# Kernel tuning notes

Measured on AMD Instinct MI355X. Metric: run time of the kernel, lower is better.

## Reference

```python
import jax, jax.numpy as jnp
import numpy as np

SEQ_LEN = 1
INPUT = 2048
HIDDEN = 2048
CLASSES = 10
K = int(np.floor(np.sqrt(HIDDEN)))            # avgKernelSize = 45
NUM_EH = (HIDDEN - K) // K + 1                # 45 pooled features
LENGTHS = (32, 128, 512)                      # EHlengths (window sizes)
EST_DIM = NUM_EH * len(LENGTHS) * 2           # mean + variance per (feature, window)
B = 8192


def setup_inputs() -> dict:
    key = jax.random.key(0)
    ks = jax.random.split(key, 7)
    s = 1.0 / np.sqrt(HIDDEN)
    u = lambda k, shape: jax.random.uniform(k, shape, jnp.float32, -s, s)
    return {
        "x": jax.random.normal(ks[0], (B, SEQ_LEN, INPUT), jnp.float32),
        "W_ih": u(ks[1], (HIDDEN, INPUT)),
        "W_hh": u(ks[2], (HIDDEN, HIDDEN)),
        "b_ih": u(ks[3], (HIDDEN,)),
        "b_hh": u(ks[4], (HIDDEN,)),
        "W_lin": u(ks[5], (CLASSES, HIDDEN + EST_DIM)),
        "b_lin": u(ks[6], (CLASSES,)),
    }


def _sliding_stats(pooled):
    """Causal sliding-window mean/variance over the batch/stream axis.

    pooled: (B, F). Returns (B, F, J, 2) with [..., 0]=mean, [..., 1]=var.
    This is the exact quantity the VarEH exponential histograms approximate
    (streaming mean/variance over the last L elements added).
    """
    n = pooled.shape[0]
    cs = jnp.cumsum(pooled, axis=0)
    cs2 = jnp.cumsum(pooled * pooled, axis=0)
    idx = jnp.arange(n)
    outs = []
    for L in LENGTHS:  # small fixed set of window lengths
        zpad = jnp.zeros((L,) + pooled.shape[1:], pooled.dtype)
        cs_l = jnp.concatenate([zpad, cs], axis=0)[:n]
        cs2_l = jnp.concatenate([zpad, cs2], axis=0)[:n]
        cnt = jnp.minimum(idx + 1, L).astype(pooled.dtype)[:, None]
        m = (cs - cs_l) / cnt
        v = (cs2 - cs2_l) / cnt - m * m
        outs.append(jnp.stack([m, v], axis=-1))  # (B, F, 2)
    return jnp.stack(outs, axis=2)  # (B, F, J, 2)


def reference(x, W_ih, W_hh, b_ih, b_hh, W_lin, b_lin):
    b = x.shape[0]
    # Elman RNN, batch_first, h0 = 0. Precompute input projection for all steps.
    xw = jnp.einsum("bsi,hi->bsh", x, W_ih) + b_ih + b_hh  # (B, S, H)

    def step(h, xt):
        h = jnp.tanh(xt + h @ W_hh.T)
        return h, h

    h0 = jnp.zeros((b, HIDDEN), x.dtype)
    _, hs = jax.lax.scan(step, h0, jnp.swapaxes(xw, 0, 1))  # (S, B, H)
    rnn_out = hs[-1]  # (B, H); with seq_len=1 this equals squeeze(rnn_out)

    # AvgPool1d(kernel=K, stride=K) over hidden dim -> (B, NUM_EH)
    pooled = rnn_out[:, : NUM_EH * K].reshape(b, NUM_EH, K).mean(axis=-1)

    # Streaming mean/var estimates across the batch stream (VarEH semantics)
    est = _sliding_stats(pooled).reshape(b, EST_DIM)

    lin_in = jnp.concatenate([rnn_out, est], axis=1)  # (B, H + EST_DIM)
    logits = lin_in @ W_lin.T + b_lin
    return jax.nn.softmax(logits, axis=1)
```

## Files before the change

### kernel.cpp

```cpp
#include <hip/hip_runtime.h>
#include <hip/hip_bf16.h>
#include <math.h>

typedef short s16x8 __attribute__((ext_vector_type(8)));
typedef float f32x4 __attribute__((ext_vector_type(4)));

__device__ inline unsigned short f2bf(float x) {
    unsigned int u = __float_as_uint(x);
    unsigned int r = (u + 0x7fffu + ((u >> 16) & 1u)) >> 16;
    return (unsigned short)r;
}
__device__ inline float bf2f(unsigned short u) {
    return __uint_as_float(((unsigned int)u) << 16);
}

__device__ inline float fast_tanh(float x) {
    float e = __expf(2.0f * x);
    return 1.0f - 2.0f * __builtin_amdgcn_rcpf(e + 1.0f);
}

__global__ void cvtprep_kernel(const float* __restrict__ x,
                               const float* __restrict__ W_ih,
                               const float* __restrict__ W_lin,
                               unsigned short* __restrict__ xb,
                               unsigned short* __restrict__ wb,
                               unsigned short* __restrict__ wlb) {
    int blk = blockIdx.x;
    int tid = threadIdx.x;
    if (blk < 16384) {
        int i = blk * 256 + tid;
        float4 v = ((const float4*)x)[i];
        ushort4 o; o.x = f2bf(v.x); o.y = f2bf(v.y); o.z = f2bf(v.z); o.w = f2bf(v.w);
        ((ushort4*)xb)[i] = o;
    } else if (blk < 20480) {
        int i = (blk - 16384) * 256 + tid;
        float4 v = ((const float4*)W_ih)[i];
        ushort4 o; o.x = f2bf(v.x); o.y = f2bf(v.y); o.z = f2bf(v.z); o.w = f2bf(v.w);
        ((ushort4*)wb)[i] = o;
    } else {
        int idx = (blk - 20480) * 256 + tid;
        if (idx < 37376) {
            int c = idx / 2336, k = idx - c * 2336;
            float v = (c < 10 && k < 2318) ? W_lin[c * 2318 + k] : 0.f;
            wlb[idx] = f2bf(v);
        }
    }
}

__global__ __launch_bounds__(256) void gemm_tanh_kernel(
    const unsigned short* __restrict__ A, const unsigned short* __restrict__ Bm,
    const float* __restrict__ b_ih, const float* __restrict__ b_hh,
    unsigned short* __restrict__ Hb)
{
    __shared__ unsigned short As[128 * 32];
    __shared__ unsigned short Bs[128 * 32];

    const int tid  = threadIdx.x;
    const int lane = tid & 63;
    const int wave = tid >> 6;
    const int row0 = blockIdx.x * 128;
    const int col0 = blockIdx.y * 128;
    const int wr = (wave >> 1) * 64;
    const int wc = (wave & 1) * 64;
    const int quad = lane >> 4;
    const int mrow = lane & 15;

    f32x4 acc[4][4];
#pragma unroll
    for (int i = 0; i < 4; ++i)
#pragma unroll
        for (int j = 0; j < 4; ++j)
            acc[i][j] = f32x4{0.f, 0.f, 0.f, 0.f};

    for (int k0 = 0; k0 < 2048; k0 += 32) {
        __syncthreads();
#pragma unroll
        for (int i = 0; i < 2; ++i) {
            int t = i * 256 + tid;
            int r = t >> 2, c = t & 3;
            int cg = c ^ ((r >> 1) & 3);
            const unsigned short* gp = A + (size_t)(row0 + r) * 2048 + k0 + cg * 8;
            __builtin_amdgcn_global_load_lds(
                (const __attribute__((address_space(1))) void*)gp,
                (__attribute__((address_space(3))) void*)(&As[t * 8]), 16, 0, 0);
        }
#pragma unroll
        for (int i = 0; i < 2; ++i) {
            int t = i * 256 + tid;
            int r = t >> 2, c = t & 3;
            int cg = c ^ ((r >> 1) & 3);
            const unsigned short* gp = Bm + (size_t)(col0 + r) * 2048 + k0 + cg * 8;
            __builtin_amdgcn_global_load_lds(
                (const __attribute__((address_space(1))) void*)gp,
                (__attribute__((address_space(3))) void*)(&Bs[t * 8]), 16, 0, 0);
        }
        __syncthreads();

        s16x8 af[4], bfr[4];
#pragma unroll
        for (int i = 0; i < 4; ++i) {
            int R = wr + i * 16 + mrow;
            int slot = quad ^ ((R >> 1) & 3);
            af[i] = *(const s16x8*)(&As[R * 32 + slot * 8]);
        }
#pragma unroll
        for (int j = 0; j < 4; ++j) {
            int R = wc + j * 16 + mrow;
            int slot = quad ^ ((R >> 1) & 3);
            bfr[j] = *(const s16x8*)(&Bs[R * 32 + slot * 8]);
        }
#pragma unroll
        for (int i = 0; i < 4; ++i)
#pragma unroll
            for (int j = 0; j < 4; ++j)
                acc[i][j] = __builtin_amdgcn_mfma_f32_16x16x32_bf16(
                    af[i], bfr[j], acc[i][j], 0, 0, 0);
    }

    float bias[4];
#pragma unroll
    for (int j = 0; j < 4; ++j) {
        int gc = col0 + wc + j * 16 + mrow;
        bias[j] = b_ih[gc] + b_hh[gc];
    }
#pragma unroll
    for (int i = 0; i < 4; ++i) {
#pragma unroll
        for (int r = 0; r < 4; ++r) {
            int grow = row0 + wr + i * 16 + quad * 4 + r;
#pragma unroll
            for (int j = 0; j < 4; ++j) {
                int gc = col0 + wc + j * 16 + mrow;
                float v = acc[i][j][r] + bias[j];
                Hb[(size_t)grow * 2048 + gc] = f2bf(fast_tanh(v));
            }
        }
    }
}

__global__ __launch_bounds__(256) void pool_kernel(
    const unsigned short* __restrict__ Hb, float* __restrict__ pooled_t) {
    __shared__ unsigned short hs[8 * 2048];
    __shared__ float outs[45 * 8];
    int b0 = blockIdx.x * 8;
    int tid = threadIdx.x;
    const ushort4* src = (const ushort4*)(Hb + (size_t)b0 * 2048);
    ushort4* dst = (ushort4*)hs;
    for (int i = tid; i < 4096; i += 256) dst[i] = src[i];
    __syncthreads();
    for (int o = tid; o < 360; o += 256) {
        int f = o % 45, r = o / 45;
        const unsigned short* row = hs + r * 2048 + f * 45;
        float s = 0.f;
#pragma unroll
        for (int k = 0; k < 45; ++k) s += bf2f(row[k]);
        outs[f * 8 + r] = s * (1.0f / 45.0f);
    }
    __syncthreads();
    for (int o = tid; o < 360; o += 256) {
        int f = o >> 3, r = o & 7;
        pooled_t[f * 8192 + b0 + r] = outs[o];
    }
}

__global__ __launch_bounds__(256) void scan_kernel(
    const float* __restrict__ pooled_t,
    float* __restrict__ cs_t, float* __restrict__ cs2_t) {
    __shared__ float t1[256], t2[256];
    int f = blockIdx.x;
    int tid = threadIdx.x;
    const float* p = pooled_t + f * 8192;
    int base = tid * 32;
    float loc[32];
    float s1 = 0.f, s2 = 0.f;
#pragma unroll
    for (int i = 0; i < 32; ++i) {
        float v = p[base + i];
        loc[i] = v; s1 += v; s2 += v * v;
    }
    t1[tid] = s1; t2[tid] = s2;
    __syncthreads();
    for (int d = 1; d < 256; d <<= 1) {
        float a1 = (tid >= d) ? t1[tid - d] : 0.f;
        float a2 = (tid >= d) ? t2[tid - d] : 0.f;
        __syncthreads();
        t1[tid] += a1; t2[tid] += a2;
        __syncthreads();
    }
    float r1 = t1[tid] - s1, r2 = t2[tid] - s2;
    float* c1 = cs_t + f * 8192;
    float* c2 = cs2_t + f * 8192;
#pragma unroll
    for (int i = 0; i < 32; ++i) {
        float v = loc[i];
        r1 += v; r2 += v * v;
        c1[base + i] = r1; c2[base + i] = r2;
    }
}

#define ESTRIDE 290
__global__ __launch_bounds__(256) void final_kernel(
    const unsigned short* __restrict__ Hb,
    const float* __restrict__ cs_t, const float* __restrict__ cs2_t,
    const unsigned short* __restrict__ Wb, const float* __restrict__ b_lin,
    float* __restrict__ out) {
    __shared__ unsigned short Es[32 * ESTRIDE];
    __shared__ float comb[2 * 16 * 17];
    int tid = threadIdx.x;
    int lane = tid & 63;
    int wave = tid >> 6;
    int b0 = blockIdx.x * 32;

    for (int i = tid; i < 135 * 32; i += 256) {
        int fj = i >> 5, r = i & 31;
        int f = fj / 3, j = fj - 3 * f;
        int b = b0 + r;
        int L = (j == 0) ? 32 : (j == 1) ? 128 : 512;
        const float* c1 = cs_t + f * 8192;
        const float* c2 = cs2_t + f * 8192;
        float a1 = c1[b], a2 = c2[b];
        float p1 = 0.f, p2 = 0.f;
        if (b >= L) { p1 = c1[b - L]; p2 = c2[b - L]; }
        float cnt = (float)((b + 1 < L) ? (b + 1) : L);
        float m = (a1 - p1) / cnt;
        float v = (a2 - p2) / cnt - m * m;
        int d0 = f * 6 + j * 2;
        Es[r * ESTRIDE + d0]     = f2bf(m);
        Es[r * ESTRIDE + d0 + 1] = f2bf(v);
    }
    for (int i = tid; i < 32 * 18; i += 256) {
        int r = i / 18, d = 270 + i % 18;
        Es[r * ESTRIDE + d] = 0;
    }
    __syncthreads();

    const int t = wave >> 1;
    const int kh = wave & 1;
    const int quad = lane >> 4;
    const int mrow = lane & 15;
    const int rowt = b0 + t * 16;

    f32x4 acc = f32x4{0.f, 0.f, 0.f, 0.f};
    const unsigned short* arow = Hb + (size_t)(rowt + mrow) * 2048 + kh * 1024 + quad * 8;
    const unsigned short* brow = Wb + (size_t)mrow * 2336 + kh * 1024 + quad * 8;
#pragma unroll 4
    for (int k = 0; k < 1024; k += 32) {
        s16x8 a = *(const s16x8*)(arow + k);
        s16x8 b = *(const s16x8*)(brow + k);
        acc = __builtin_amdgcn_mfma_f32_16x16x32_bf16(a, b, acc, 0, 0, 0);
    }
    if (kh) {
        const unsigned short* erow = Es + (t * 16 + mrow) * ESTRIDE + quad * 8;
        const unsigned short* wrow = Wb + (size_t)mrow * 2336 + 2048 + quad * 8;
#pragma unroll
        for (int k = 0; k < 288; k += 32) {
            s16x8 a = *(const s16x8*)(erow + k);
            s16x8 b = *(const s16x8*)(wrow + k);
            acc = __builtin_amdgcn_mfma_f32_16x16x32_bf16(a, b, acc, 0, 0, 0);
        }
    }

    float* cb = comb + t * 272;
    if (kh == 0) {
#pragma unroll
        for (int r = 0; r < 4; ++r) cb[(quad * 4 + r) * 17 + mrow] = acc[r];
    }
    __syncthreads();
    if (kh == 1) {
#pragma unroll
        for (int r = 0; r < 4; ++r) cb[(quad * 4 + r) * 17 + mrow] += acc[r];
    }
    __syncthreads();

    if (tid < 32) {
        const float* base = comb + (tid >> 4) * 272 + (tid & 15) * 17;
        float lg[10];
        float mx = -1e30f;
#pragma unroll
        for (int c = 0; c < 10; ++c) {
            lg[c] = base[c] + b_lin[c];
            mx = fmaxf(mx, lg[c]);
        }
        float s = 0.f;
#pragma unroll
        for (int c = 0; c < 10; ++c) { lg[c] = expf(lg[c] - mx); s += lg[c]; }
        float inv = 1.0f / s;
#pragma unroll
        for (int c = 0; c < 10; ++c) out[(size_t)(b0 + tid) * 10 + c] = lg[c] * inv;
    }
}

extern "C" void kernel_launch(void* const* d_in, const int* in_sizes, int n_in,
                              void* d_out, int out_size, void* d_ws, size_t ws_size,
                              hipStream_t stream) {
    const float* x     = (const float*)d_in[0];
    const float* W_ih  = (const float*)d_in[1];
    const float* b_ih  = (const float*)d_in[3];
    const float* b_hh  = (const float*)d_in[4];
    const float* W_lin = (const float*)d_in[5];
    const float* b_lin = (const float*)d_in[6];
    float* out = (float*)d_out;

    char* ws = (char*)d_ws;
    unsigned short* xb  = (unsigned short*)(ws);
    unsigned short* wb  = (unsigned short*)(ws + 33554432);
    unsigned short* Hb  = (unsigned short*)(ws + 41943040);
    float* pooled_t     = (float*)(ws + 75497472);
    float* cs_t         = (float*)(ws + 76972032);
    float* cs2_t        = (float*)(ws + 78446592);
    unsigned short* wlb = (unsigned short*)(ws + 79921152);

    cvtprep_kernel<<<20626, 256, 0, stream>>>(x, W_ih, W_lin, xb, wb, wlb);
    dim3 ggrid(64, 16);
    gemm_tanh_kernel<<<ggrid, 256, 0, stream>>>(xb, wb, b_ih, b_hh, Hb);
    pool_kernel<<<1024, 256, 0, stream>>>(Hb, pooled_t);
    scan_kernel<<<45, 256, 0, stream>>>(pooled_t, cs_t, cs2_t);
    final_kernel<<<256, 256, 0, stream>>>(Hb, cs_t, cs2_t, wlb, b_lin, out);
}
```

Baseline: 253.8 us.

## Fuse fp32-to-bf16 conversion of x into the GEMM load path

Removes the separate pass that converted the 64MB fp32 input x to bf16 in workspace. The GEMM now loads fp32 x directly into registers, converts to bf16 and stores to LDS, while W_ih is still pre-converted. The grid is transposed so the 16 column blocks sharing the same rows of x run adjacently, which improves L2 reuse of the now twice-as-large fp32 A tiles. The cost is synchronous register-staged loads instead of async global_load_lds, plus conversion ALU work inside the main loop.

```diff
diff --git a/kernel.cpp b/kernel.cpp
--- a/kernel.cpp
+++ b/kernel.cpp
@@ -10,6 +10,9 @@
     unsigned int r = (u + 0x7fffu + ((u >> 16) & 1u)) >> 16;
     return (unsigned short)r;
 }
+__device__ inline unsigned int f2bf2(float lo, float hi) {
+    return ((unsigned int)f2bf(hi) << 16) | (unsigned int)f2bf(lo);
+}
 __device__ inline float bf2f(unsigned short u) {
     return __uint_as_float(((unsigned int)u) << 16);
 }
@@ -19,26 +22,19 @@
     return 1.0f - 2.0f * __builtin_amdgcn_rcpf(e + 1.0f);
 }
 
-__global__ void cvtprep_kernel(const float* __restrict__ x,
-                               const float* __restrict__ W_ih,
-                               const float* __restrict__ W_lin,
-                               unsigned short* __restrict__ xb,
-                               unsigned short* __restrict__ wb,
-                               unsigned short* __restrict__ wlb) {
+__global__ void prep_kernel(const float* __restrict__ W_ih,
+                            const float* __restrict__ W_lin,
+                            unsigned short* __restrict__ wb,
+                            unsigned short* __restrict__ wlb) {
     int blk = blockIdx.x;
     int tid = threadIdx.x;
-    if (blk < 16384) {
+    if (blk < 4096) {
         int i = blk * 256 + tid;
-        float4 v = ((const float4*)x)[i];
-        ushort4 o; o.x = f2bf(v.x); o.y = f2bf(v.y); o.z = f2bf(v.z); o.w = f2bf(v.w);
-        ((ushort4*)xb)[i] = o;
-    } else if (blk < 20480) {
-        int i = (blk - 16384) * 256 + tid;
         float4 v = ((const float4*)W_ih)[i];
         ushort4 o; o.x = f2bf(v.x); o.y = f2bf(v.y); o.z = f2bf(v.z); o.w = f2bf(v.w);
         ((ushort4*)wb)[i] = o;
     } else {
-        int idx = (blk - 20480) * 256 + tid;
+        int idx = (blk - 4096) * 256 + tid;
         if (idx < 37376) {
             int c = idx / 2336, k = idx - c * 2336;
             float v = (c < 10 && k < 2318) ? W_lin[c * 2318 + k] : 0.f;
@@ -48,7 +44,7 @@
 }
 
 __global__ __launch_bounds__(256) void gemm_tanh_kernel(
-    const unsigned short* __restrict__ A, const unsigned short* __restrict__ Bm,
+    const float* __restrict__ Ax, const unsigned short* __restrict__ Bm,
     const float* __restrict__ b_ih, const float* __restrict__ b_hh,
     unsigned short* __restrict__ Hb)
 {
@@ -58,8 +54,8 @@
     const int tid  = threadIdx.x;
     const int lane = tid & 63;
     const int wave = tid >> 6;
-    const int row0 = blockIdx.x * 128;
-    const int col0 = blockIdx.y * 128;
+    const int col0 = blockIdx.x * 128;
+    const int row0 = blockIdx.y * 128;
     const int wr = (wave >> 1) * 64;
     const int wc = (wave & 1) * 64;
     const int quad = lane >> 4;
@@ -73,16 +69,26 @@
             acc[i][j] = f32x4{0.f, 0.f, 0.f, 0.f};
 
     for (int k0 = 0; k0 < 2048; k0 += 32) {
+        float4 fa[2][2];
+#pragma unroll
+        for (int i = 0; i < 2; ++i) {
+            int c = i * 256 + tid;
+            int r = c >> 2, c4 = c & 3;
+            int cg = c4 ^ ((r >> 1) & 3);
+            const float* gp = Ax + (size_t)(row0 + r) * 2048 + k0 + cg * 8;
+            fa[i][0] = *(const float4*)gp;
+            fa[i][1] = *(const float4*)(gp + 4);
+        }
         __syncthreads();
 #pragma unroll
         for (int i = 0; i < 2; ++i) {
-            int t = i * 256 + tid;
-            int r = t >> 2, c = t & 3;
-            int cg = c ^ ((r >> 1) & 3);
-            const unsigned short* gp = A + (size_t)(row0 + r) * 2048 + k0 + cg * 8;
-            __builtin_amdgcn_global_load_lds(
-                (const __attribute__((address_space(1))) void*)gp,
-                (__attribute__((address_space(3))) void*)(&As[t * 8]), 16, 0, 0);
+            int c = i * 256 + tid;
+            uint4 q;
+            q.x = f2bf2(fa[i][0].x, fa[i][0].y);
+            q.y = f2bf2(fa[i][0].z, fa[i][0].w);
+            q.z = f2bf2(fa[i][1].x, fa[i][1].y);
+            q.w = f2bf2(fa[i][1].z, fa[i][1].w);
+            *(uint4*)(&As[c * 8]) = q;
         }
 #pragma unroll
         for (int i = 0; i < 2; ++i) {
@@ -273,12 +279,12 @@
     __syncthreads();
 
     if (tid < 32) {
-        const float* base = comb + (tid >> 4) * 272 + (tid & 15) * 17;
+        const float* basep = comb + (tid >> 4) * 272 + (tid & 15) * 17;
         float lg[10];
         float mx = -1e30f;
 #pragma unroll
         for (int c = 0; c < 10; ++c) {
-            lg[c] = base[c] + b_lin[c];
+            lg[c] = basep[c] + b_lin[c];
             mx = fmaxf(mx, lg[c]);
         }
         float s = 0.f;
@@ -302,17 +308,16 @@
     float* out = (float*)d_out;
 
     char* ws = (char*)d_ws;
-    unsigned short* xb  = (unsigned short*)(ws);
-    unsigned short* wb  = (unsigned short*)(ws + 33554432);
-    unsigned short* Hb  = (unsigned short*)(ws + 41943040);
-    float* pooled_t     = (float*)(ws + 75497472);
-    float* cs_t         = (float*)(ws + 76972032);
-    float* cs2_t        = (float*)(ws + 78446592);
-    unsigned short* wlb = (unsigned short*)(ws + 79921152);
-
-    cvtprep_kernel<<<20626, 256, 0, stream>>>(x, W_ih, W_lin, xb, wb, wlb);
-    dim3 ggrid(64, 16);
-    gemm_tanh_kernel<<<ggrid, 256, 0, stream>>>(xb, wb, b_ih, b_hh, Hb);
+    unsigned short* wb  = (unsigned short*)(ws);
+    unsigned short* Hb  = (unsigned short*)(ws + 8388608);
+    float* pooled_t     = (float*)(ws + 41943040);
+    float* cs_t         = (float*)(ws + 43417600);
+    float* cs2_t        = (float*)(ws + 44892160);
+    unsigned short* wlb = (unsigned short*)(ws + 46366720);
+
+    prep_kernel<<<4243, 256, 0, stream>>>(W_ih, W_lin, wb, wlb);
+    dim3 ggrid(16, 64);
+    gemm_tanh_kernel<<<ggrid, 256, 0, stream>>>(x, wb, b_ih, b_hh, Hb);
     pool_kernel<<<1024, 256, 0, stream>>>(Hb, pooled_t);
     scan_kernel<<<45, 256, 0, stream>>>(pooled_t, cs_t, cs2_t);
     final_kernel<<<256, 256, 0, stream>>>(Hb, cs_t, cs2_t, wlb, b_lin, out);
```

After: 309.7 us. 1.22x slower.

## Fuse average pooling into GEMM-tanh epilogue with atomic partial sums

Applied to the files above, without the earlier changes.

Removes the separate pool kernel. The GEMM epilogue now stages each 64-column half of the tanh output tile in shared memory, sums the pooling windows that overlap it, and atomically adds partial means into pooled_t. The prep kernel zeroes pooled_t first. This saves one launch and a full re-read of the 32 MB Hb buffer, at the cost of extra barriers, serialized epilogue halves, float atomics with nondeterministic summation order, and more shared memory.

```diff
diff --git a/kernel.cpp b/kernel.cpp
--- a/kernel.cpp
+++ b/kernel.cpp
@@ -19,12 +19,13 @@
     return 1.0f - 2.0f * __builtin_amdgcn_rcpf(e + 1.0f);
 }
 
-__global__ void cvtprep_kernel(const float* __restrict__ x,
-                               const float* __restrict__ W_ih,
-                               const float* __restrict__ W_lin,
-                               unsigned short* __restrict__ xb,
-                               unsigned short* __restrict__ wb,
-                               unsigned short* __restrict__ wlb) {
+__global__ void prep_kernel(const float* __restrict__ x,
+                            const float* __restrict__ W_ih,
+                            const float* __restrict__ W_lin,
+                            unsigned short* __restrict__ xb,
+                            unsigned short* __restrict__ wb,
+                            unsigned short* __restrict__ wlb,
+                            float* __restrict__ pooled_t) {
     int blk = blockIdx.x;
     int tid = threadIdx.x;
     if (blk < 16384) {
@@ -37,23 +38,28 @@
         float4 v = ((const float4*)W_ih)[i];
         ushort4 o; o.x = f2bf(v.x); o.y = f2bf(v.y); o.z = f2bf(v.z); o.w = f2bf(v.w);
         ((ushort4*)wb)[i] = o;
-    } else {
+    } else if (blk < 20626) {
         int idx = (blk - 20480) * 256 + tid;
         if (idx < 37376) {
             int c = idx / 2336, k = idx - c * 2336;
             float v = (c < 10 && k < 2318) ? W_lin[c * 2318 + k] : 0.f;
             wlb[idx] = f2bf(v);
         }
+    } else {
+        int idx = (blk - 20626) * 256 + tid;
+        ((float4*)pooled_t)[idx] = float4{0.f, 0.f, 0.f, 0.f};
     }
 }
 
 __global__ __launch_bounds__(256) void gemm_tanh_kernel(
     const unsigned short* __restrict__ A, const unsigned short* __restrict__ Bm,
     const float* __restrict__ b_ih, const float* __restrict__ b_hh,
-    unsigned short* __restrict__ Hb)
+    unsigned short* __restrict__ Hb, float* __restrict__ pooled_t)
 {
-    __shared__ unsigned short As[128 * 32];
-    __shared__ unsigned short Bs[128 * 32];
+    __shared__ unsigned short sbuf[8448];
+    unsigned short* As = sbuf;
+    unsigned short* Bs = sbuf + 4096;
+    unsigned short* Ps = sbuf;
 
     const int tid  = threadIdx.x;
     const int lane = tid & 63;
@@ -123,43 +129,48 @@
         int gc = col0 + wc + j * 16 + mrow;
         bias[j] = b_ih[gc] + b_hh[gc];
     }
-#pragma unroll
-    for (int i = 0; i < 4; ++i) {
-#pragma unroll
-        for (int r = 0; r < 4; ++r) {
-            int grow = row0 + wr + i * 16 + quad * 4 + r;
-#pragma unroll
-            for (int j = 0; j < 4; ++j) {
-                int gc = col0 + wc + j * 16 + mrow;
-                float v = acc[i][j][r] + bias[j];
-                Hb[(size_t)grow * 2048 + gc] = f2bf(fast_tanh(v));
+
+#pragma unroll 1
+    for (int p = 0; p < 2; ++p) {
+        __syncthreads();
+        if ((wc >> 6) == p) {
+#pragma unroll
+            for (int i = 0; i < 4; ++i) {
+#pragma unroll
+                for (int r = 0; r < 4; ++r) {
+                    int lrow = wr + i * 16 + quad * 4 + r;
+                    int grow = row0 + lrow;
+#pragma unroll
+                    for (int j = 0; j < 4; ++j) {
+                        int lcol = j * 16 + mrow;
+                        float v = acc[i][j][r] + bias[j];
+                        unsigned short h = f2bf(fast_tanh(v));
+                        Hb[(size_t)grow * 2048 + col0 + wc + lcol] = h;
+                        Ps[lrow * 66 + lcol] = h;
+                    }
+                }
             }
         }
-    }
-}
-
-__global__ __launch_bounds__(256) void pool_kernel(
-    const unsigned short* __restrict__ Hb, float* __restrict__ pooled_t) {
-    __shared__ unsigned short hs[8 * 2048];
-    __shared__ float outs[45 * 8];
-    int b0 = blockIdx.x * 8;
-    int tid = threadIdx.x;
-    const ushort4* src = (const ushort4*)(Hb + (size_t)b0 * 2048);
-    ushort4* dst = (ushort4*)hs;
-    for (int i = tid; i < 4096; i += 256) dst[i] = src[i];
-    __syncthreads();
-    for (int o = tid; o < 360; o += 256) {
-        int f = o % 45, r = o / 45;
-        const unsigned short* row = hs + r * 2048 + f * 45;
-        float s = 0.f;
-#pragma unroll
-        for (int k = 0; k < 45; ++k) s += bf2f(row[k]);
-        outs[f * 8 + r] = s * (1.0f / 45.0f);
-    }
-    __syncthreads();
-    for (int o = tid; o < 360; o += 256) {
-        int f = o >> 3, r = o & 7;
-        pooled_t[f * 8192 + b0 + r] = outs[o];
+        __syncthreads();
+        int c0 = col0 + p * 64;
+        int f0 = c0 / 45;
+        int f1 = (c0 + 63) / 45; if (f1 > 44) f1 = 44;
+        int nf = f1 - f0 + 1;
+        int ntask = 128 * nf;
+        for (int t = tid; t < ntask; t += 256) {
+            int row = t / nf;
+            int f = f0 + (t - row * nf);
+            int clo = f * 45; if (clo < c0) clo = c0;
+            int chi = f * 45 + 45;
+            if (chi > c0 + 64) chi = c0 + 64;
+            if (chi > 2025) chi = 2025;
+            if (chi > clo) {
+                float s = 0.f;
+                for (int c = clo; c < chi; ++c)
+                    s += bf2f(Ps[row * 66 + (c - c0)]);
+                atomicAdd(&pooled_t[f * 8192 + row0 + row], s * (1.0f / 45.0f));
+            }
+        }
     }
 }
 
@@ -273,12 +284,12 @@
     __syncthreads();
 
     if (tid < 32) {
-        const float* base = comb + (tid >> 4) * 272 + (tid & 15) * 17;
+        const float* basep = comb + (tid >> 4) * 272 + (tid & 15) * 17;
         float lg[10];
         float mx = -1e30f;
 #pragma unroll
         for (int c = 0; c < 10; ++c) {
-            lg[c] = base[c] + b_lin[c];
+            lg[c] = basep[c] + b_lin[c];
             mx = fmaxf(mx, lg[c]);
         }
         float s = 0.f;
@@ -310,10 +321,9 @@
     float* cs2_t        = (float*)(ws + 78446592);
     unsigned short* wlb = (unsigned short*)(ws + 79921152);
 
-    cvtprep_kernel<<<20626, 256, 0, stream>>>(x, W_ih, W_lin, xb, wb, wlb);
+    prep_kernel<<<20986, 256, 0, stream>>>(x, W_ih, W_lin, xb, wb, wlb, pooled_t);
     dim3 ggrid(64, 16);
-    gemm_tanh_kernel<<<ggrid, 256, 0, stream>>>(xb, wb, b_ih, b_hh, Hb);
-    pool_kernel<<<1024, 256, 0, stream>>>(Hb, pooled_t);
+    gemm_tanh_kernel<<<ggrid, 256, 0, stream>>>(xb, wb, b_ih, b_hh, Hb, pooled_t);
     scan_kernel<<<45, 256, 0, stream>>>(pooled_t, cs_t, cs2_t);
     final_kernel<<<256, 256, 0, stream>>>(Hb, cs_t, cs2_t, wlb, b_lin, out);
 }
```

After: 253.9 us. No clear change (+0.0%).
